# Optimization experiments

Hardware: AMD Instinct MI355X
Metric: run time of the kernel (lower is better)

Reference implementation:

```python
import jax, jax.numpy as jnp
import numpy as np
from jax import lax

CW = 8       # current_window
PW = 8       # pretrain_window
HEADS = 8
LOG100 = float(np.log(100.0))


def setup_inputs() -> dict:
    key = jax.random.key(0)
    ks = jax.random.split(key, 8)
    B, H, W, C = 8, 126, 126, 256
    f32 = jnp.float32
    return {
        "x": jax.random.normal(ks[0], (B, H, W, C), f32),
        "w_qkv": jax.random.normal(ks[1], (C, 3 * C), f32) * 0.02,      # 1x1 conv, no bias
        "w_dw": jax.random.normal(ks[2], (3, 3, 1, 3 * C), f32) * 0.1,  # depthwise 3x3, HWIO
        "ln_gamma": jnp.ones((3 * C,), f32),
        "ln_beta": jnp.zeros((3 * C,), f32),
        "q_bias": jnp.zeros((C,), f32),
        "v_bias": jnp.zeros((C,), f32),
        "scale": jnp.full((HEADS, 1, 1), np.log(10.0), f32),
        "cpb_w0": jax.random.normal(ks[3], (2, 512), f32) * 0.02,
        "cpb_b0": jnp.zeros((512,), f32),
        "cpb_w1": jax.random.normal(ks[4], (512, HEADS), f32) * 0.02,   # no bias, sigmoid
        "w_proj": jax.random.normal(ks[5], (C, C), f32) * 0.02,
    }


def _l2n(t):
    # tf.math.l2_normalize with epsilon=1.55e-5
    return t * lax.rsqrt(jnp.maximum(jnp.sum(t * t, axis=-1, keepdims=True), 1.55e-5))


def _cpb_bias(cpb_w0, cpb_b0, cpb_w1, cw, L, heads):
    # log-spaced continuous relative position table (static)
    rel = np.arange(1 - cw, cw, dtype=np.float32)
    rel = np.stack(np.meshgrid(rel, rel, indexing='ij'), axis=-1)  # [2cw-1, 2cw-1, 2]
    rel = rel * (8.0 / (PW - 1.0))
    rel = np.sign(rel) * np.log1p(np.abs(rel)) / np.log(8.0)
    ri = np.arange(cw)
    ri = np.stack(np.meshgrid(ri, ri, indexing='ij'), axis=0).reshape(2, -1)
    ri = ri[:, :, None] - ri[:, None, :] + (cw - 1)
    relidx = (ri[0] * (2 * cw - 1) + ri[1]).reshape(-1)  # [L*L]
    h = jax.nn.relu(jnp.asarray(rel.reshape(-1, 2)) @ cpb_w0 + cpb_b0)
    bias = jax.nn.sigmoid(h @ cpb_w1) * 16.0             # [(2cw-1)^2, heads]
    bias = bias[jnp.asarray(relidx)].reshape(L, L, heads)
    return bias.transpose(2, 0, 1)                        # [heads, L, L]


def reference(x, w_qkv, w_dw, ln_gamma, ln_beta, q_bias, v_bias, scale,
              cpb_w0, cpb_b0, cpb_w1, w_proj):
    B, H, W, C = x.shape
    cw, heads = CW, HEADS
    hd = C // heads
    L = cw * cw

    # qkv 1x1 conv + depthwise 3x3 + layernorm (ConvNorm)
    qkv = jnp.einsum('bhwc,cd->bhwd', x, w_qkv)           # [B,H,W,3C]
    qkv = lax.conv_general_dilated(qkv, w_dw, (1, 1), 'SAME',
                                   dimension_numbers=('NHWC', 'HWIO', 'NHWC'),
                                   feature_group_count=3 * C)
    mu = jnp.mean(qkv, axis=-1, keepdims=True)
    var = jnp.mean(jnp.square(qkv - mu), axis=-1, keepdims=True)
    qkv = (qkv - mu) * lax.rsqrt(var + 1e-5) * ln_gamma + ln_beta
    qkv = qkv + jnp.concatenate([q_bias, jnp.zeros_like(q_bias), v_bias])

    # pad to multiple of window, grid-partition (MaxViT-style strided grid)
    pad_h, pad_w = (-H) % cw, (-W) % cw
    hb, wb = pad_h // 2, pad_w // 2
    qkv = jnp.pad(qkv, ((0, 0), (hb, pad_h - hb), (wb, pad_w - wb), (0, 0)))
    Hp, Wp = H + pad_h, W + pad_w
    Hb, Wb = Hp // cw, Wp // cw
    nw = Hb * Wb
    qkv = qkv.reshape(B, cw, Hb, cw, Wb, 3, heads, hd)
    qkv = qkv.transpose(0, 2, 4, 6, 1, 3, 5, 7).reshape(B * nw, heads, L, 3, hd)
    q, k, v = qkv[..., 0, :], qkv[..., 1, :], qkv[..., 2, :]

    # cosine attention with learned per-head log-scale (clamped at log 100)
    q, k = _l2n(q), _l2n(k)
    ls = jnp.exp(jnp.minimum(scale, LOG100))              # [heads,1,1]
    attn = jnp.einsum('nhqd,nhkd->nhqk', q * ls, k)

    attn = attn + _cpb_bias(cpb_w0, cpb_b0, cpb_w1, cw, L, heads)[None]

    if pad_h + pad_w > 0:
        m = jnp.pad(jnp.ones((1, H, W, 1), attn.dtype),
                    ((0, 0), (hb, pad_h - hb), (wb, pad_w - wb), (0, 0)))
        m = m.reshape(1, cw, Hb, cw, Wb, 1).transpose(0, 2, 4, 1, 3, 5).reshape(nw, L)
        mbias = -100.0 * (m == 0).astype(attn.dtype)       # [nw, L] over keys
        attn = attn.reshape(B, nw, heads, L, L) + mbias[None, :, None, None, :]
        attn = attn.reshape(B * nw, heads, L, L)

    attn = jax.nn.softmax(attn, axis=-1)
    out = jnp.einsum('nhqk,nhkd->nhqd', attn, v)           # [B*nw, heads, L, hd]

    # reverse grid partition + crop + projection
    out = out.reshape(B, Hb, Wb, heads, cw, cw, hd)
    out = out.transpose(0, 4, 1, 5, 2, 3, 6).reshape(B, Hp, Wp, C)
    out = out[:, hb:hb + H, wb:wb + W]
    return jnp.einsum('bhwc,cd->bhwd', out, w_proj)
```

## Files before the change

kernel.cpp:

```cpp
#include <hip/hip_runtime.h>

typedef unsigned short ushort;
typedef __bf16 bf16x8 __attribute__((ext_vector_type(8)));
typedef float f32x4 __attribute__((ext_vector_type(4)));
typedef float f4 __attribute__((ext_vector_type(4)));
typedef unsigned short us8 __attribute__((ext_vector_type(8)));
typedef unsigned short us4 __attribute__((ext_vector_type(4)));
typedef unsigned u32x4v __attribute__((ext_vector_type(4)));

#define NPIX 127008
#define HDIM 126
#define WDIM 126

__device__ __forceinline__ float bf2f(ushort u) {
  unsigned v = ((unsigned)u) << 16;
  return __builtin_bit_cast(float, v);
}
__device__ __forceinline__ ushort f2bf(float f) {
  unsigned x = __builtin_bit_cast(unsigned, f);
  x += 0x7fffu + ((x >> 16) & 1u);
  return (ushort)(x >> 16);
}

__global__ void k_cvt_x(const float* __restrict__ x, ushort* __restrict__ xb, int n8) {
  const int stride = gridDim.x * blockDim.x;
  for (int i = blockIdx.x * blockDim.x + threadIdx.x; i < n8; i += stride) {
    const f4 a = *(const f4*)&x[(size_t)i * 8];
    const f4 b = *(const f4*)&x[(size_t)i * 8 + 4];
    us8 o;
#pragma unroll
    for (int j = 0; j < 4; ++j) { o[j] = f2bf(a[j]); o[4 + j] = f2bf(b[j]); }
    *(us8*)&xb[(size_t)i * 8] = o;
  }
}

__global__ void k_cvt_wT(const float* __restrict__ in, ushort* __restrict__ out, int N, int K) {
  const int t = blockIdx.x * 256 + threadIdx.x;
  const int n = t / K, k = t - n * K;
  out[t] = f2bf(in[(size_t)k * N + n]);
}

__device__ __forceinline__ float frel(int i) {
  const float v = (float)(i - 7) * (8.0f / 7.0f);
  const float a = log1pf(fabsf(v)) * 0.4808983469629878f;
  return v < 0.f ? -a : a;
}

__global__ __launch_bounds__(256) void k_cpb1(const float* __restrict__ w0,
    const float* __restrict__ b0, const float* __restrict__ w1, float* __restrict__ tmp) {
  const int p = blockIdx.x * 4 + (threadIdx.x >> 6);
  const int lane = threadIdx.x & 63;
  if (p >= 225) return;
  const float r0 = frel(p / 15), r1 = frel(p % 15);
  float hv[8];
#pragma unroll
  for (int jj = 0; jj < 8; ++jj) {
    const int j = lane * 8 + jj;
    hv[jj] = fmaxf(0.f, r0 * w0[j] + r1 * w0[512 + j] + b0[j]);
  }
  for (int h = 0; h < 8; ++h) {
    float part = 0.f;
#pragma unroll
    for (int jj = 0; jj < 8; ++jj) part += hv[jj] * w1[(lane * 8 + jj) * 8 + h];
    for (int o = 32; o; o >>= 1) part += __shfl_xor(part, o);
    if (lane == 0) tmp[p * 8 + h] = 16.f / (1.f + __expf(-part));
  }
}

__global__ void k_cpb2(const float* __restrict__ tmp, float* __restrict__ biasV) {
  const int t = blockIdx.x * 256 + threadIdx.x;
  const int h = t >> 12, rest = t & 4095;
  const int ki = rest >> 10, g = (rest >> 8) & 3, q = (rest >> 2) & 63, r = rest & 3;
  const int key = ki * 16 + g * 4 + r;
  const int d0 = (q >> 3) - (key >> 3) + 7, d1 = (q & 7) - (key & 7) + 7;
  biasV[t] = tmp[(d0 * 15 + d1) * 8 + h];
}

#define GLL(g, l) __builtin_amdgcn_global_load_lds( \
    (const __attribute__((address_space(1))) void*)(g), \
    (__attribute__((address_space(3))) void*)(l), 16, 0, 0)

template <int OUTF, int NX>
__global__ __launch_bounds__(256) void k_gemm(const ushort* __restrict__ A,
                                              const ushort* __restrict__ Bt,
                                              void* __restrict__ Cv, int M, int N) {
  constexpr int K = 256;
  __shared__ ushort lsA[128 * 32];
  __shared__ ushort lsB[128 * 32];
  const int tid = threadIdx.x;
  const int wid = tid >> 6, lane = tid & 63;

  const int nwg = gridDim.x;
  const int q8 = nwg >> 3, r8 = nwg & 7;
  const int xcd = blockIdx.x & 7, pos = blockIdx.x >> 3;
  const int lin = (xcd < r8) ? xcd * (q8 + 1) + pos
                             : r8 * (q8 + 1) + (xcd - r8) * q8 + pos;
  const int m0 = (lin / NX) * 128, n0 = (lin % NX) * 128;

  f32x4 acc[4][4];
#pragma unroll
  for (int i = 0; i < 4; ++i)
#pragma unroll
    for (int j = 0; j < 4; ++j) acc[i][j] = 0.f;

  const int srow = tid >> 2, sk = (tid & 3) * 8;
  const int aw = (wid >> 1) * 64, bw = (wid & 1) * 64;
  const int fr = lane & 15, kg = (lane >> 4) * 8;
  char* lA = (char*)lsA + wid * 1024;
  char* lB = (char*)lsB + wid * 1024;

  int ra0 = m0 + srow;      if (ra0 >= M) ra0 = M - 1;
  int ra1 = m0 + srow + 64; if (ra1 >= M) ra1 = M - 1;
  const int rb0 = n0 + srow, rb1 = n0 + srow + 64;

  for (int kt = 0; kt < K; kt += 32) {
    __syncthreads();
    GLL(A + (size_t)ra0 * K + kt + sk, lA);
    GLL(A + (size_t)ra1 * K + kt + sk, lA + 4096);
    GLL(Bt + (size_t)rb0 * K + kt + sk, lB);
    GLL(Bt + (size_t)rb1 * K + kt + sk, lB + 4096);
    __syncthreads();
    bf16x8 af[4], bb[4];
#pragma unroll
    for (int i = 0; i < 4; ++i)
      af[i] = *(const bf16x8*)&lsA[(aw + i * 16 + fr) * 32 + kg];
#pragma unroll
    for (int j = 0; j < 4; ++j)
      bb[j] = *(const bf16x8*)&lsB[(bw + j * 16 + fr) * 32 + kg];
#pragma unroll
    for (int i = 0; i < 4; ++i)
#pragma unroll
      for (int j = 0; j < 4; ++j)
        acc[i][j] = __builtin_amdgcn_mfma_f32_16x16x32_bf16(af[i], bb[j], acc[i][j], 0, 0, 0);
  }

  const int r4 = (lane >> 4) * 4, cc = lane & 15;
#pragma unroll
  for (int i = 0; i < 4; ++i) {
#pragma unroll
    for (int j = 0; j < 4; ++j) {
      const int gc = n0 + bw + j * 16 + cc;
#pragma unroll
      for (int r = 0; r < 4; ++r) {
        const int gr = m0 + aw + i * 16 + r4 + r;
        if (gr < M) {
          if constexpr (OUTF == 0)
            ((ushort*)Cv)[(size_t)gr * N + gc] = f2bf(acc[i][j][r]);
          else
            ((float*)Cv)[(size_t)gr * N + gc] = acc[i][j][r];
        }
      }
    }
  }
}

__global__ __launch_bounds__(256) void k_convw(const ushort* __restrict__ pre,
    const float* __restrict__ wdw, ushort* __restrict__ qkvw) {
  const int nwg = gridDim.x;
  const int q8 = nwg >> 3, r8 = nwg & 7;
  const int xcd = blockIdx.x & 7, pos = blockIdx.x >> 3;
  const int lin = (xcd < r8) ? xcd * (q8 + 1) + pos
                             : r8 * (q8 + 1) + (xcd - r8) * q8 + pos;
  const int t = lin * 256 + threadIdx.x;
  const int chunk = t % 192;
  const int rs = t / 192;
  const int rowid = rs % 1008;
  const int seg = rs / 1008;
  const int b = rowid / HDIM, h = rowid - b * HDIM;
  const int c0 = chunk * 4;

  float wt[9][4];
#pragma unroll
  for (int tap = 0; tap < 9; ++tap) {
    const f4 wa = *(const f4*)&wdw[tap * 768 + c0];
#pragma unroll
    for (int j = 0; j < 4; ++j) wt[tap][j] = wa[j];
  }
  if (h == 0) {
#pragma unroll
    for (int tap = 0; tap < 3; ++tap)
#pragma unroll
      for (int j = 0; j < 4; ++j) wt[tap][j] = 0.f;
  }
  if (h == HDIM - 1) {
#pragma unroll
    for (int tap = 6; tap < 9; ++tap)
#pragma unroll
      for (int j = 0; j < 4; ++j) wt[tap][j] = 0.f;
  }

  const int hm = h > 0 ? h - 1 : 0, hp2 = h < HDIM - 1 ? h + 1 : HDIM - 1;
  const ushort* r0 = pre + (size_t)((b * HDIM + hm) * WDIM) * 768 + c0;
  const ushort* r1 = pre + (size_t)((b * HDIM + h) * WDIM) * 768 + c0;
  const ushort* r2 = pre + (size_t)((b * HDIM + hp2) * WDIM) * 768 + c0;

  const int w0 = seg * 18;
  float b0_[3][4], b1_[3][4], b2_[3][4], b3_[3][4];

#define LOADCOL(dst, w)                                                   \
  {                                                                       \
    us4 u0 = *(const us4*)&r0[(size_t)(w) * 768];                         \
    us4 u1 = *(const us4*)&r1[(size_t)(w) * 768];                         \
    us4 u2 = *(const us4*)&r2[(size_t)(w) * 768];                         \
    _Pragma("unroll") for (int j = 0; j < 4; ++j) {                       \
      dst[0][j] = bf2f(u0[j]); dst[1][j] = bf2f(u1[j]); dst[2][j] = bf2f(u2[j]); } \
  }
#define ZEROCOL(dst)                                                      \
  { _Pragma("unroll") for (int rr = 0; rr < 3; ++rr)                      \
    _Pragma("unroll") for (int j = 0; j < 4; ++j) dst[rr][j] = 0.f; }

  if (w0 > 0) { LOADCOL(b0_, w0 - 1) } else { ZEROCOL(b0_) }
  LOADCOL(b1_, w0)
  LOADCOL(b2_, w0 + 1)

  const int dstc = ((b << 8) + (((h + 1) & 15) << 4)) << 6;
  const int dsth = ((h + 1) >> 4) << 3;

#define BODY(L, C, R, P, w)                                               \
  {                                                                       \
    if ((w) + 2 < WDIM) { LOADCOL(P, (w) + 2) } else { ZEROCOL(P) }       \
    float acc[4];                                                         \
    _Pragma("unroll") for (int j = 0; j < 4; ++j)                         \
      acc[j] = L[0][j] * wt[0][j] + C[0][j] * wt[1][j] + R[0][j] * wt[2][j] \
             + L[1][j] * wt[3][j] + C[1][j] * wt[4][j] + R[1][j] * wt[5][j] \
             + L[2][j] * wt[6][j] + C[2][j] * wt[7][j] + R[2][j] * wt[8][j]; \
    const int wp = (w) + 1;                                               \
    const int dstrow = dstc + ((wp & 15) << 6) + dsth + (wp >> 4);        \
    us4 o;                                                                \
    _Pragma("unroll") for (int j = 0; j < 4; ++j) o[j] = f2bf(acc[j]);    \
    *(us4*)&qkvw[(size_t)dstrow * 768 + c0] = o;                          \
  }

#pragma unroll 1
  for (int w = w0; w < w0 + 16; w += 4) {
    BODY(b0_, b1_, b2_, b3_, w)
    BODY(b1_, b2_, b3_, b0_, w + 1)
    BODY(b2_, b3_, b0_, b1_, w + 2)
    BODY(b3_, b0_, b1_, b2_, w + 3)
  }
  BODY(b0_, b1_, b2_, b3_, w0 + 16)
  BODY(b1_, b2_, b3_, b0_, w0 + 17)
#undef BODY
#undef LOADCOL
#undef ZEROCOL
}

__global__ __launch_bounds__(256) void k_ln2(ushort* __restrict__ qkvw,
    const float* __restrict__ gamma, const float* __restrict__ beta,
    const float* __restrict__ qb, const float* __restrict__ vb,
    const float* __restrict__ scale) {
  const int pix = blockIdx.x * 4 + (threadIdx.x >> 6);
  const int lane = threadIdx.x & 63;
  const int w = pix % WDIM, t2 = pix / WDIM, h = t2 % HDIM, b = t2 / HDIM;
  const int hp = h + 1, wp = w + 1;
  const int dstrow = (((b << 8) + ((hp & 15) << 4) + (wp & 15)) << 6) + ((hp >> 4) << 3) + (wp >> 4);
  ushort* row = qkvw + (size_t)dstrow * 768;

  float v[3][4];
#pragma unroll
  for (int c = 0; c < 3; ++c) {
    const us4 u = *(const us4*)&row[(lane + 64 * c) * 4];
#pragma unroll
    for (int j = 0; j < 4; ++j) v[c][j] = bf2f(u[j]);
  }
  float s = 0.f;
#pragma unroll
  for (int c = 0; c < 3; ++c)
#pragma unroll
    for (int j = 0; j < 4; ++j) s += v[c][j];
  for (int o = 32; o; o >>= 1) s += __shfl_xor(s, o);
  const float mu = s * (1.f / 768.f);
  float ss = 0.f;
#pragma unroll
  for (int c = 0; c < 3; ++c)
#pragma unroll
    for (int j = 0; j < 4; ++j) { const float d = v[c][j] - mu; ss += d * d; }
  for (int o = 32; o; o >>= 1) ss += __shfl_xor(ss, o);
  const float rs = rsqrtf(ss * (1.f / 768.f) + 1e-5f);

  float y[3][4];
#pragma unroll
  for (int c = 0; c < 3; ++c) {
    const int chb = (lane + 64 * c) * 4;
#pragma unroll
    for (int j = 0; j < 4; ++j)
      y[c][j] = (v[c][j] - mu) * rs * gamma[chb + j] + beta[chb + j];
  }
#pragma unroll
  for (int j = 0; j < 4; ++j) { y[0][j] += qb[lane * 4 + j]; y[2][j] += vb[lane * 4 + j]; }

#pragma unroll
  for (int c = 0; c < 2; ++c) {
    float g = y[c][0] * y[c][0] + y[c][1] * y[c][1] + y[c][2] * y[c][2] + y[c][3] * y[c][3];
    g += __shfl_xor(g, 1); g += __shfl_xor(g, 2); g += __shfl_xor(g, 4);
    const float rn = rsqrtf(fmaxf(g, 1.55e-5f));
#pragma unroll
    for (int j = 0; j < 4; ++j) y[c][j] *= rn;
  }
  const float ls = __expf(fminf(scale[lane >> 3], 4.60517025f));
#pragma unroll
  for (int j = 0; j < 4; ++j) y[0][j] *= ls;

#pragma unroll
  for (int c = 0; c < 3; ++c) {
    us4 u;
#pragma unroll
    for (int j = 0; j < 4; ++j) u[j] = f2bf(y[c][j]);
    *(us4*)&row[(lane + 64 * c) * 4] = u;
  }
}

__global__ __launch_bounds__(256) void k_attn(const ushort* __restrict__ qkvw,
    const float* __restrict__ biasV, ushort* __restrict__ aout) {
  __shared__ ushort Vs[4][64][36];
  const int wid = threadIdx.x >> 6, lane = threadIdx.x & 63;
  const int u = blockIdx.x * 4 + wid;
  const int head = u >> 11, wl = u & 2047;
  const int b = wl >> 8, wh = (wl >> 4) & 15, ww = wl & 15;
  const int c = lane & 15, g = lane >> 4;
  const int g4 = g * 4, g8 = g * 8;
  const ushort* wb = qkvw + (size_t)wl * 64 * 768;
  const us8 zz = 0;

  const bool e_r0 = (wh == 0), e_r7 = (wh == 15), e_c0 = (ww == 0), e_c7 = (ww == 15);
#define TOKVALID(t) (!(((e_r0) & (((t) >> 3) == 0)) | ((e_r7) & (((t) >> 3) == 7)) | \
                       ((e_c0) & (((t) & 7) == 0)) | ((e_c7) & (((t) & 7) == 7))))

  {
    const bool tv = TOKVALID(lane);
    const ushort* vp = wb + (size_t)lane * 768 + 512 + head * 32;
    us8 v0 = *(const us8*)vp;
    us8 v1 = *(const us8*)(vp + 8);
    us8 v2 = *(const us8*)(vp + 16);
    us8 v3 = *(const us8*)(vp + 24);
    v0 = tv ? v0 : zz;
    v1 = tv ? v1 : zz;
    v2 = tv ? v2 : zz;
    v3 = tv ? v3 : zz;
    ushort* vr = &Vs[wid][lane][0];
    *(us4*)&vr[0]  = __builtin_shufflevector(v0, v0, 0, 1, 2, 3);
    *(us4*)&vr[4]  = __builtin_shufflevector(v0, v0, 4, 5, 6, 7);
    *(us4*)&vr[8]  = __builtin_shufflevector(v1, v1, 0, 1, 2, 3);
    *(us4*)&vr[12] = __builtin_shufflevector(v1, v1, 4, 5, 6, 7);
    *(us4*)&vr[16] = __builtin_shufflevector(v2, v2, 0, 1, 2, 3);
    *(us4*)&vr[20] = __builtin_shufflevector(v2, v2, 4, 5, 6, 7);
    *(us4*)&vr[24] = __builtin_shufflevector(v3, v3, 0, 1, 2, 3);
    *(us4*)&vr[28] = __builtin_shufflevector(v3, v3, 4, 5, 6, 7);
  }

  bf16x8 kf[4], qf[4];
#pragma unroll
  for (int ki = 0; ki < 4; ++ki) {
    const int tk = ki * 16 + c;
    us8 kv = *(const us8*)&wb[(size_t)tk * 768 + 256 + head * 32 + g8];
    kv = TOKVALID(tk) ? kv : zz;
    kf[ki] = __builtin_bit_cast(bf16x8, kv);
  }
#pragma unroll
  for (int qj = 0; qj < 4; ++qj) {
    const int tq = qj * 16 + c;
    us8 qv = *(const us8*)&wb[(size_t)tq * 768 + head * 32 + g8];
    qv = TOKVALID(tq) ? qv : zz;
    qf[qj] = __builtin_bit_cast(bf16x8, qv);
  }

  const float* bvh = biasV + (head << 12);
  f32x4 st[4][4];
#pragma unroll
  for (int ki = 0; ki < 4; ++ki)
#pragma unroll
    for (int qj = 0; qj < 4; ++qj) {
      const f32x4 bfrag = *(const f32x4*)&bvh[((ki * 4 + g) << 8) + ((qj * 16 + c) << 2)];
      st[ki][qj] = __builtin_amdgcn_mfma_f32_16x16x32_bf16(kf[ki], qf[qj], bfrag, 0, 0, 0);
    }

  unsigned afr[4][2][4];
#pragma unroll
  for (int qj = 0; qj < 4; ++qj) {
    float s[16];
#pragma unroll
    for (int ki = 0; ki < 4; ++ki)
#pragma unroll
      for (int r = 0; r < 4; ++r) {
        const int key = ki * 16 + g4 + r;
        s[ki * 4 + r] = TOKVALID(key) ? st[ki][qj][r] : -1e30f;
      }
    float m = s[0];
#pragma unroll
    for (int i = 1; i < 16; ++i) m = fmaxf(m, s[i]);
    m = fmaxf(m, __shfl_xor(m, 16));
    m = fmaxf(m, __shfl_xor(m, 32));
    float den = 0.f;
#pragma unroll
    for (int i = 0; i < 16; ++i) { s[i] = __expf(s[i] - m); den += s[i]; }
    den += __shfl_xor(den, 16);
    den += __shfl_xor(den, 32);
    const float inv = 1.f / den;

    unsigned pk[4][2];
#pragma unroll
    for (int ki = 0; ki < 4; ++ki) {
      pk[ki][0] = ((unsigned)f2bf(s[ki * 4 + 1] * inv) << 16) | f2bf(s[ki * 4 + 0] * inv);
      pk[ki][1] = ((unsigned)f2bf(s[ki * 4 + 3] * inv) << 16) | f2bf(s[ki * 4 + 2] * inv);
    }
#pragma unroll
    for (int j2 = 0; j2 < 4; ++j2) {
      const int src = c + 16 * (2 * (g & 1) + (j2 >> 1));
      const unsigned s0 = __shfl(pk[0][j2 & 1], src);
      const unsigned s1 = __shfl(pk[1][j2 & 1], src);
      const unsigned s2 = __shfl(pk[2][j2 & 1], src);
      const unsigned s3 = __shfl(pk[3][j2 & 1], src);
      afr[qj][0][j2] = (g < 2) ? s0 : s1;
      afr[qj][1][j2] = (g < 2) ? s2 : s3;
    }
  }

  f32x4 ao[4][2];
#pragma unroll
  for (int qi = 0; qi < 4; ++qi)
#pragma unroll
    for (int di = 0; di < 2; ++di) ao[qi][di] = 0.f;
#pragma unroll
  for (int kc = 0; kc < 2; ++kc) {
#pragma unroll
    for (int di = 0; di < 2; ++di) {
      us8 bv;
#pragma unroll
      for (int j = 0; j < 8; ++j) bv[j] = Vs[wid][kc * 32 + g8 + j][di * 16 + c];
      const bf16x8 bb = __builtin_bit_cast(bf16x8, bv);
#pragma unroll
      for (int qi = 0; qi < 4; ++qi) {
        const u32x4v aw4 = {afr[qi][kc][0], afr[qi][kc][1], afr[qi][kc][2], afr[qi][kc][3]};
        ao[qi][di] = __builtin_amdgcn_mfma_f32_16x16x32_bf16(
            __builtin_bit_cast(bf16x8, aw4), bb, ao[qi][di], 0, 0, 0);
      }
    }
  }

#pragma unroll
  for (int qi = 0; qi < 4; ++qi)
#pragma unroll
    for (int r = 0; r < 4; ++r) {
      const int q = qi * 16 + g4 + r;
      if (TOKVALID(q)) {
        const int h = (q >> 3) * 16 + wh - 1, w2 = (q & 7) * 16 + ww - 1;
        ushort* op = aout + ((size_t)((b * HDIM + h) * WDIM + w2)) * 256 + head * 32;
        op[c] = f2bf(ao[qi][0][r]);
        op[16 + c] = f2bf(ao[qi][1][r]);
      }
    }
#undef TOKVALID
}

extern "C" void kernel_launch(void* const* d_in, const int* in_sizes, int n_in,
                              void* d_out, int out_size, void* d_ws, size_t ws_size,
                              hipStream_t stream) {
  (void)in_sizes; (void)n_in; (void)out_size; (void)ws_size;
  const float* x      = (const float*)d_in[0];
  const float* w_qkv  = (const float*)d_in[1];
  const float* w_dw   = (const float*)d_in[2];
  const float* ln_g   = (const float*)d_in[3];
  const float* ln_b   = (const float*)d_in[4];
  const float* q_bias = (const float*)d_in[5];
  const float* v_bias = (const float*)d_in[6];
  const float* scale  = (const float*)d_in[7];
  const float* cpb_w0 = (const float*)d_in[8];
  const float* cpb_b0 = (const float*)d_in[9];
  const float* cpb_w1 = (const float*)d_in[10];
  const float* w_proj = (const float*)d_in[11];
  float* out = (float*)d_out;

  char* ws = (char*)d_ws;
  const size_t PRE  = (size_t)NPIX * 768 * 2;
  const size_t QKVW = (size_t)131072 * 768 * 2;
  ushort* pre    = (ushort*)ws;
  ushort* qkvw   = (ushort*)(ws + PRE);
  ushort* xb     = (ushort*)(ws + PRE);
  ushort* aoutb  = pre;
  ushort* wqkvT  = (ushort*)(ws + PRE + QKVW);
  ushort* wprojT = (ushort*)(ws + PRE + QKVW + (size_t)768 * 256 * 2);
  float*  cpbtmp = (float*)(ws + PRE + QKVW + (size_t)768 * 256 * 2 + (size_t)256 * 256 * 2);
  float*  biasV  = (float*)(ws + PRE + QKVW + (size_t)768 * 256 * 2 + (size_t)256 * 256 * 2 + 8192);

  k_cvt_wT<<<768, 256, 0, stream>>>(w_qkv, wqkvT, 768, 256);
  k_cvt_wT<<<256, 256, 0, stream>>>(w_proj, wprojT, 256, 256);
  k_cpb1<<<57, 256, 0, stream>>>(cpb_w0, cpb_b0, cpb_w1, cpbtmp);
  k_cpb2<<<128, 256, 0, stream>>>(cpbtmp, biasV);
  k_cvt_x<<<2048, 256, 0, stream>>>(x, xb, NPIX * 256 / 8);
  k_gemm<0, 6><<<5958, 256, 0, stream>>>(xb, wqkvT, pre, NPIX, 768);
  k_convw<<<5292, 256, 0, stream>>>(pre, w_dw, qkvw);
  k_ln2<<<31752, 256, 0, stream>>>(qkvw, ln_g, ln_b, q_bias, v_bias, scale);
  k_attn<<<4096, 256, 0, stream>>>(qkvw, biasV, aoutb);
  k_gemm<1, 2><<<1986, 256, 0, stream>>>(aoutb, wprojT, out, NPIX, 256);
}
```

Measured before the change: 501.0 us.

## Fuse layernorm, biases and q/k l2-normalisation into depthwise conv kernel

Merges the separate layernorm kernel into the depthwise 3x3 conv kernel. Each 192-thread block now handles one full row of 768 channels, so per-pixel mean and variance come from wave shuffles plus a small shared-memory reduction. This removes a full bf16 write, re-read and write pass over the 131072x768 qkv buffer. In exchange it adds two block barriers per output pixel, uses a one-pass variance formula (E[x^2]-mu^2) with some precision risk, and runs smaller blocks.

```diff
diff --git a/kernel.cpp b/kernel.cpp
--- a/kernel.cpp
+++ b/kernel.cpp
@@ -154,19 +154,22 @@
   }
 }
 
-__global__ __launch_bounds__(256) void k_convw(const ushort* __restrict__ pre,
-    const float* __restrict__ wdw, ushort* __restrict__ qkvw) {
+__global__ __launch_bounds__(192) void k_convln(const ushort* __restrict__ pre,
+    const float* __restrict__ wdw,
+    const float* __restrict__ gamma, const float* __restrict__ beta,
+    const float* __restrict__ qb, const float* __restrict__ vb,
+    const float* __restrict__ scale, ushort* __restrict__ qkvw) {
+  __shared__ float red[3][2];
   const int nwg = gridDim.x;
   const int q8 = nwg >> 3, r8 = nwg & 7;
   const int xcd = blockIdx.x & 7, pos = blockIdx.x >> 3;
   const int lin = (xcd < r8) ? xcd * (q8 + 1) + pos
                              : r8 * (q8 + 1) + (xcd - r8) * q8 + pos;
-  const int t = lin * 256 + threadIdx.x;
-  const int chunk = t % 192;
-  const int rs = t / 192;
-  const int rowid = rs % 1008;
-  const int seg = rs / 1008;
+  const int rowid = lin % 1008;
+  const int seg = lin / 1008;
   const int b = rowid / HDIM, h = rowid - b * HDIM;
+  const int chunk = threadIdx.x;
+  const int wid = chunk >> 6, lane = chunk & 63;
   const int c0 = chunk * 4;
 
   float wt[9][4];
@@ -188,6 +191,13 @@
 #pragma unroll
       for (int j = 0; j < 4; ++j) wt[tap][j] = 0.f;
   }
+
+  const f4 g4 = *(const f4*)&gamma[c0];
+  const f4 b4 = *(const f4*)&beta[c0];
+  f4 addb = {0.f, 0.f, 0.f, 0.f};
+  if (wid == 0) addb = *(const f4*)&qb[c0];
+  if (wid == 2) addb = *(const f4*)&vb[c0 - 512];
+  const float ls = (wid == 0) ? __expf(fminf(scale[chunk >> 3], 4.60517025f)) : 1.f;
 
   const int hm = h > 0 ? h - 1 : 0, hp2 = h < HDIM - 1 ? h + 1 : HDIM - 1;
   const ushort* r0 = pre + (size_t)((b * HDIM + hm) * WDIM) * 768 + c0;
@@ -224,10 +234,32 @@
       acc[j] = L[0][j] * wt[0][j] + C[0][j] * wt[1][j] + R[0][j] * wt[2][j] \
              + L[1][j] * wt[3][j] + C[1][j] * wt[4][j] + R[1][j] * wt[5][j] \
              + L[2][j] * wt[6][j] + C[2][j] * wt[7][j] + R[2][j] * wt[8][j]; \
+            \
+    float s_ = acc[0] + acc[1] + acc[2] + acc[3];                         \
+    float ss_ = acc[0]*acc[0] + acc[1]*acc[1] + acc[2]*acc[2] + acc[3]*acc[3]; \
+    _Pragma("unroll") for (int o = 32; o; o >>= 1) {                      \
+      s_ += __shfl_xor(s_, o); ss_ += __shfl_xor(ss_, o); }               \
+    if (lane == 0) { red[wid][0] = s_; red[wid][1] = ss_; }               \
+    __syncthreads();                                                      \
+    const float tot = red[0][0] + red[1][0] + red[2][0];                  \
+    const float tot2 = red[0][1] + red[1][1] + red[2][1];                 \
+    __syncthreads();                                                      \
+    const float mu = tot * (1.f / 768.f);                                 \
+    const float var = tot2 * (1.f / 768.f) - mu * mu;                     \
+    const float rs = rsqrtf(var + 1e-5f);                                 \
+    float y[4];                                                           \
+    _Pragma("unroll") for (int j = 0; j < 4; ++j)                         \
+      y[j] = (acc[j] - mu) * rs * g4[j] + b4[j] + addb[j];                \
+    if (wid < 2) {      \
+      float gg = y[0]*y[0] + y[1]*y[1] + y[2]*y[2] + y[3]*y[3];           \
+      gg += __shfl_xor(gg, 1); gg += __shfl_xor(gg, 2); gg += __shfl_xor(gg, 4); \
+      const float rn = rsqrtf(fmaxf(gg, 1.55e-5f)) * ls;                  \
+      _Pragma("unroll") for (int j = 0; j < 4; ++j) y[j] *= rn;           \
+    }                                                                     \
     const int wp = (w) + 1;                                               \
     const int dstrow = dstc + ((wp & 15) << 6) + dsth + (wp >> 4);        \
     us4 o;                                                                \
-    _Pragma("unroll") for (int j = 0; j < 4; ++j) o[j] = f2bf(acc[j]);    \
+    _Pragma("unroll") for (int j = 0; j < 4; ++j) o[j] = f2bf(y[j]);      \
     *(us4*)&qkvw[(size_t)dstrow * 768 + c0] = o;                          \
   }
 
@@ -243,71 +275,6 @@
 #undef BODY
 #undef LOADCOL
 #undef ZEROCOL
-}
-
-__global__ __launch_bounds__(256) void k_ln2(ushort* __restrict__ qkvw,
-    const float* __restrict__ gamma, const float* __restrict__ beta,
-    const float* __restrict__ qb, const float* __restrict__ vb,
-    const float* __restrict__ scale) {
-  const int pix = blockIdx.x * 4 + (threadIdx.x >> 6);
-  const int lane = threadIdx.x & 63;
-  const int w = pix % WDIM, t2 = pix / WDIM, h = t2 % HDIM, b = t2 / HDIM;
-  const int hp = h + 1, wp = w + 1;
-  const int dstrow = (((b << 8) + ((hp & 15) << 4) + (wp & 15)) << 6) + ((hp >> 4) << 3) + (wp >> 4);
-  ushort* row = qkvw + (size_t)dstrow * 768;
-
-  float v[3][4];
-#pragma unroll
-  for (int c = 0; c < 3; ++c) {
-    const us4 u = *(const us4*)&row[(lane + 64 * c) * 4];
-#pragma unroll
-    for (int j = 0; j < 4; ++j) v[c][j] = bf2f(u[j]);
-  }
-  float s = 0.f;
-#pragma unroll
-  for (int c = 0; c < 3; ++c)
-#pragma unroll
-    for (int j = 0; j < 4; ++j) s += v[c][j];
-  for (int o = 32; o; o >>= 1) s += __shfl_xor(s, o);
-  const float mu = s * (1.f / 768.f);
-  float ss = 0.f;
-#pragma unroll
-  for (int c = 0; c < 3; ++c)
-#pragma unroll
-    for (int j = 0; j < 4; ++j) { const float d = v[c][j] - mu; ss += d * d; }
-  for (int o = 32; o; o >>= 1) ss += __shfl_xor(ss, o);
-  const float rs = rsqrtf(ss * (1.f / 768.f) + 1e-5f);
-
-  float y[3][4];
-#pragma unroll
-  for (int c = 0; c < 3; ++c) {
-    const int chb = (lane + 64 * c) * 4;
-#pragma unroll
-    for (int j = 0; j < 4; ++j)
-      y[c][j] = (v[c][j] - mu) * rs * gamma[chb + j] + beta[chb + j];
-  }
-#pragma unroll
-  for (int j = 0; j < 4; ++j) { y[0][j] += qb[lane * 4 + j]; y[2][j] += vb[lane * 4 + j]; }
-
-#pragma unroll
-  for (int c = 0; c < 2; ++c) {
-    float g = y[c][0] * y[c][0] + y[c][1] * y[c][1] + y[c][2] * y[c][2] + y[c][3] * y[c][3];
-    g += __shfl_xor(g, 1); g += __shfl_xor(g, 2); g += __shfl_xor(g, 4);
-    const float rn = rsqrtf(fmaxf(g, 1.55e-5f));
-#pragma unroll
-    for (int j = 0; j < 4; ++j) y[c][j] *= rn;
-  }
-  const float ls = __expf(fminf(scale[lane >> 3], 4.60517025f));
-#pragma unroll
-  for (int j = 0; j < 4; ++j) y[0][j] *= ls;
-
-#pragma unroll
-  for (int c = 0; c < 3; ++c) {
-    us4 u;
-#pragma unroll
-    for (int j = 0; j < 4; ++j) u[j] = f2bf(y[c][j]);
-    *(us4*)&row[(lane + 64 * c) * 4] = u;
-  }
 }
 
 __global__ __launch_bounds__(256) void k_attn(const ushort* __restrict__ qkvw,
@@ -488,8 +455,7 @@
   k_cpb2<<<128, 256, 0, stream>>>(cpbtmp, biasV);
   k_cvt_x<<<2048, 256, 0, stream>>>(x, xb, NPIX * 256 / 8);
   k_gemm<0, 6><<<5958, 256, 0, stream>>>(xb, wqkvT, pre, NPIX, 768);
-  k_convw<<<5292, 256, 0, stream>>>(pre, w_dw, qkvw);
-  k_ln2<<<31752, 256, 0, stream>>>(qkvw, ln_g, ln_b, q_bias, v_bias, scale);
+  k_convln<<<7056, 192, 0, stream>>>(pre, w_dw, ln_g, ln_b, q_bias, v_bias, scale, qkvw);
   k_attn<<<4096, 256, 0, stream>>>(qkvw, biasV, aoutb);
   k_gemm<1, 2><<<1986, 256, 0, stream>>>(aoutb, wprojT, out, NPIX, 256);
 }
```

Measured after the change: 488.3 us. -2.5%, faster.
